# Kernel optimization log

Hardware: AMD Instinct MI355X
Metric: run time of the kernel (lower is better)

## Reference

```python
import jax, jax.numpy as jnp
import numpy as np

B, T, F, N = 262144, 3, 17, 8
EMBD = 32
DT = 0.2  # 25/5*0.04
EPS = 1e-8  # torch.cosine_similarity eps


def _mono(x, wi, bi, wo, bo):
    # monotonic_fun with increasing=False: relu(-Linear(x)) -> Linear
    h = jax.nn.relu(-(x @ wi.T + bi))  # (..., EMBD)
    return h @ wo.T + bo               # (..., 1)


def _cos(a, b):
    dot = jnp.sum(a * b, axis=-1)
    na = jnp.maximum(jnp.linalg.norm(a, axis=-1), EPS)
    nb = jnp.maximum(jnp.linalg.norm(b, axis=-1), EPS)
    return dot / (na * nb)


def _angle_clamp(vec, e, ang):
    # vec: (B,K,2), e: (B,2) -> keep forces within effective angle cone, sum over K
    keep = jnp.abs(_cos(e[:, None, :], vec)) > ang
    return jnp.sum(vec * keep[..., None], axis=1)


def setup_inputs() -> dict:
    key = jax.random.key(0)
    ks = jax.random.split(key, 8)
    ego = jax.random.normal(ks[0], (B, T, F), jnp.float32)
    ego = ego.at[:, :, 2:4].multiply(10.0)  # position scale
    nei = jax.random.normal(ks[1], (B, N, F), jnp.float32)
    nei = nei.at[:, :, 2:4].multiply(10.0).at[:, :, 4:6].multiply(0.1)
    border = jax.random.normal(ks[2], (4,), jnp.float32)
    attr_dest_para = jax.random.uniform(ks[3], (2,), jnp.float32) + 0.1  # relu(rand), keep away from 0 divisor
    eff_angle = jax.nn.sigmoid(jax.random.uniform(ks[4], (1,), jnp.float32))

    def mlp(k):
        k1, k2, k3, k4 = jax.random.split(k, 4)
        wi = jax.random.uniform(k1, (EMBD, 1), jnp.float32)      # clamped >= 0
        bi = jax.random.normal(k2, (EMBD,), jnp.float32) * 0.1
        wo = jax.random.uniform(k3, (1, EMBD), jnp.float32) * 0.1  # clamped >= 0
        bo = jax.random.normal(k4, (1,), jnp.float32) * 0.1
        return wi, bi, wo, bo

    an = mlp(ks[5])
    rn = mlp(ks[6])
    rb = mlp(ks[7])
    dl = mlp(jax.random.fold_in(key, 99))
    return dict(
        ego=ego, nei=nei, border=border,
        attr_dest_para=attr_dest_para, eff_angle=eff_angle,
        an_wi=an[0], an_bi=an[1], an_wo=an[2], an_bo=an[3],
        rn_wi=rn[0], rn_bi=rn[1], rn_wo=rn[2], rn_bo=rn[3],
        rb_wi=rb[0], rb_bi=rb[1], rb_wo=rb[2], rb_bo=rb[3],
        dl_wi=dl[0], dl_bi=dl[1], dl_wo=dl[2], dl_bo=dl[3],
    )


def reference(ego, nei, border, attr_dest_para, eff_angle,
              an_wi, an_bi, an_wo, an_bo,
              rn_wi, rn_bi, rn_wo, rn_bo,
              rb_wi, rb_bi, rb_wo, rb_bo,
              dl_wi, dl_bi, dl_wo, dl_bo):
    ego_last = ego[:, -1]  # (B,F)

    # --- attr_destination (desired_velocity=None branch) ---
    v34 = ego_last[:, 3:5]
    dv = jnp.stack([jnp.linalg.norm(v34, axis=-1),
                    jnp.zeros(ego.shape[0], ego.dtype)], axis=1)  # (B,2)
    f_dest = ((attr_dest_para[1] * dv - v34) / attr_dest_para[0])[:, None, :]  # (B,1,2)

    # --- attr_repu_neighbors ---
    r = nei[:, :, 2:4] - ego_last[:, None, 2:4]  # (B,N,2)
    mask = nei[:, :, 2:4] == 0                    # (B,N,2)
    r_norm = jnp.linalg.norm(r, axis=-1, keepdims=True)  # (B,N,1)

    # neighbor durality: quirky use of batch element 1, shared across batch
    ids_last = ego[1, -1, 8:-1]  # (8,) neighbor-id columns
    dur = jnp.zeros(N, ego.dtype)
    for t in range(ego.shape[1]):
        dur = dur + jnp.isin(ids_last, ego[1, t, 8:-1]).astype(ego.dtype)

    f_attr = _mono(r_norm, an_wi, an_bi, an_wo, an_bo) * r / r_norm \
             * _mono(dur[:, None], dl_wi, dl_bi, dl_wo, dl_bo)  # (B,N,2)*(N,1)
    f_attr = jnp.where(mask, 0.0, f_attr)

    v_nei = nei[:, :, 4:6]
    b = r_norm \
        + jnp.sum((r + v_nei * DT) ** 2, axis=-1, keepdims=True) \
        - jnp.sum((v_nei * DT) ** 2, axis=-1, keepdims=True)
    b = jnp.sqrt(b) / 2
    f_repu = _mono(b, rn_wi, rn_bi, rn_wo, rn_bo) * r / r_norm
    f_repu = jnp.where(mask, 0.0, f_repu)

    # --- repu_borders (select_lane = [0, -1]) ---
    rb_all = ego_last[:, 3, None] - border        # (B,4)
    rbv = jnp.stack([rb_all[:, 0], rb_all[:, -1]], axis=1)  # (B,2)
    rbn = jnp.abs(rbv)
    f_bor = _mono(rbn[..., None], rb_wi, rb_bi, rb_wo, rb_bo) * (rbv / rbn)[..., None]  # (B,2,1)
    f_bor = jnp.concatenate([jnp.zeros_like(f_bor), f_bor], axis=-1)  # (B,2,2): [0, fy]

    # --- angle clamp + integrate ---
    e = ego_last[:, 4:6]
    e = e / jnp.linalg.norm(e, axis=1, keepdims=True)
    a = (_angle_clamp(f_dest, e, eff_angle)
         + _angle_clamp(f_attr, e, eff_angle) + _angle_clamp(f_repu, e, eff_angle)
         + _angle_clamp(f_bor, e, eff_angle))
    v = ego_last[:, 2:4] + a * DT
    s = ego_last[:, :2] + v * DT
    return jnp.concatenate([s, v, a], axis=1)  # (B,6)
```

## Files before the change

### kernel.cpp

```cpp
#include <hip/hip_runtime.h>

#define DTC 0.2f
#define EPSC 1e-8f

__global__ void sfm_pre(const float* __restrict__ ego,
                        const float* __restrict__ dl_wi,
                        const float* __restrict__ dl_bi,
                        const float* __restrict__ dl_wo,
                        const float* __restrict__ dl_bo,
                        float* __restrict__ ws) {
    int t = threadIdx.x;
    int j = t >> 5, k = t & 31;
    const float* base = ego + 51;
    float idv = base[2 * 17 + 8 + j];
    float dur = 0.f;
    for (int tt = 0; tt < 3; ++tt) {
        bool f = false;
        for (int m = 0; m < 8; ++m) f = f || (idv == base[tt * 17 + 8 + m]);
        dur += f ? 1.f : 0.f;
    }
    float part = dl_wo[k] * fmaxf(0.f, -fmaf(dl_wi[k], dur, dl_bi[k]));
#pragma unroll
    for (int m = 1; m < 32; m <<= 1) part += __shfl_xor(part, m, 64);
    if (k == 0) ws[j] = part + dl_bo[0];
}

__global__ __launch_bounds__(256) void sfm_main(
    const float* __restrict__ ego, const float* __restrict__ nei,
    const float* __restrict__ border, const float* __restrict__ adp,
    const float* __restrict__ eang,
    const float* __restrict__ an_wi, const float* __restrict__ an_bi,
    const float* __restrict__ an_wo, const float* __restrict__ an_bo,
    const float* __restrict__ rn_wi, const float* __restrict__ rn_bi,
    const float* __restrict__ rn_wo, const float* __restrict__ rn_bo,
    const float* __restrict__ rb_wi, const float* __restrict__ rb_bi,
    const float* __restrict__ rb_wo, const float* __restrict__ rb_bo,
    const float* __restrict__ dlf,
    float* __restrict__ out, int Bn)
{
    __shared__ float sw[304];
    int t = threadIdx.x;
    if (t < 32) {
        sw[t]        = an_wi[t]; sw[32 + t]  = an_bi[t]; sw[64 + t]  = an_wo[t];
        sw[96 + t]   = rn_wi[t]; sw[128 + t] = rn_bi[t]; sw[160 + t] = rn_wo[t];
        sw[192 + t]  = rb_wi[t]; sw[224 + t] = rb_bi[t]; sw[256 + t] = rb_wo[t];
    }
    if (t >= 32 && t < 40) sw[288 + (t - 32)] = dlf[t - 32];
    if (t == 40) sw[296] = an_bo[0];
    if (t == 41) sw[297] = rn_bo[0];
    if (t == 42) sw[298] = rb_bo[0];
    if (t == 43) sw[299] = adp[0];
    if (t == 44) sw[300] = adp[1];
    if (t == 45) sw[301] = eang[0];
    if (t == 46) sw[302] = border[0];
    if (t == 47) sw[303] = border[3];
    __syncthreads();

    int l = t & 7;
    long long row = (long long)blockIdx.x * 32 + (t >> 3);
    if (row >= Bn) return;

    float egv = 0.f;
    if (l < 6) egv = ego[row * 51 + 34 + l];
    int lb = (t & 63) & ~7;
    float g0 = __shfl(egv, lb + 0, 64);
    float g1 = __shfl(egv, lb + 1, 64);
    float g2 = __shfl(egv, lb + 2, 64);
    float g3 = __shfl(egv, lb + 3, 64);
    float g4 = __shfl(egv, lb + 4, 64);
    float g5 = __shfl(egv, lb + 5, 64);

    const float* nr = nei + row * 136 + l * 17 + 2;
    float nx = nr[0], ny = nr[1], vx = nr[2], vy = nr[3];

    float Rx = nx - g2, Ry = ny - g3;
    float rr = sqrtf(Rx * Rx + Ry * Ry);
    float ax = fmaf(vx, DTC, Rx), ay = fmaf(vy, DTC, Ry);
    float wx = vx * DTC, wy = vy * DTC;
    float bb = sqrtf(rr + ax * ax + ay * ay - wx * wx - wy * wy) * 0.5f;

    float rb0 = g3 - sw[302], rb1 = g3 - sw[303];
    float rbn0 = fabsf(rb0), rbn1 = fabsf(rb1);

    float accA = 0.f, accR = 0.f;
#pragma unroll 8
    for (int k = 0; k < 32; ++k) {
        float h = fmaxf(0.f, -fmaf(sw[k], rr, sw[32 + k]));
        accA = fmaf(sw[64 + k], h, accA);
        float g = fmaxf(0.f, -fmaf(sw[96 + k], bb, sw[128 + k]));
        accR = fmaf(sw[160 + k], g, accR);
    }
    float pB0 = 0.f, pB1 = 0.f;
#pragma unroll
    for (int m = 0; m < 4; ++m) {
        int k = l + 8 * m;
        float bwi = sw[192 + k], bbi = sw[224 + k], bwo = sw[256 + k];
        pB0 = fmaf(bwo, fmaxf(0.f, -fmaf(bwi, rbn0, bbi)), pB0);
        pB1 = fmaf(bwo, fmaxf(0.f, -fmaf(bwi, rbn1, bbi)), pB1);
    }

    float an_bo_v = sw[296], rn_bo_v = sw[297], rb_bo_v = sw[298];
    float p0 = sw[299], p1 = sw[300], ang = sw[301];

    float elen = sqrtf(g4 * g4 + g5 * g5);
    float ex = g4 / elen, ey = g5 / elen;
    float na = fmaxf(sqrtf(ex * ex + ey * ey), EPSC);

    float axs = 0.f, ays = 0.f;
#define CLAMP_ADD(VX, VY)                                                   \
    {                                                                       \
        float _vx = (VX), _vy = (VY);                                       \
        float _nv = fmaxf(sqrtf(_vx * _vx + _vy * _vy), EPSC);              \
        float _c = (ex * _vx + ey * _vy) / (na * _nv);                      \
        if (fabsf(_c) > ang) { axs += _vx; ays += _vy; }                    \
    }

    float mfx = (nx == 0.f) ? 0.f : 1.f;
    float mfy = (ny == 0.f) ? 0.f : 1.f;

    {
        float coef = (accA + an_bo_v) / rr * sw[288 + l];
        CLAMP_ADD(coef * Rx * mfx, coef * Ry * mfy);
    }
    {
        float coef = (accR + rn_bo_v) / rr;
        CLAMP_ADD(coef * Rx * mfx, coef * Ry * mfy);
    }

#pragma unroll
    for (int m = 1; m < 8; m <<= 1) {
        axs += __shfl_xor(axs, m, 64);
        ays += __shfl_xor(ays, m, 64);
        pB0 += __shfl_xor(pB0, m, 64);
        pB1 += __shfl_xor(pB1, m, 64);
    }

    if (l == 0) {
        float dvn = sqrtf(g3 * g3 + g4 * g4);
        CLAMP_ADD((p1 * dvn - g3) / p0, -g4 / p0);
        float f0 = (pB0 + rb_bo_v) * (rb0 / rbn0);
        float f1 = (pB1 + rb_bo_v) * (rb1 / rbn1);
        CLAMP_ADD(0.f, f0);
        CLAMP_ADD(0.f, f1);

        float vxo = fmaf(axs, DTC, g2);
        float vyo = fmaf(ays, DTC, g3);
        float* op = out + row * 6;
        op[0] = fmaf(vxo, DTC, g0);
        op[1] = fmaf(vyo, DTC, g1);
        op[2] = vxo; op[3] = vyo;
        op[4] = axs; op[5] = ays;
    }
#undef CLAMP_ADD
}

extern "C" void kernel_launch(void* const* d_in, const int* in_sizes, int n_in,
                              void* d_out, int out_size, void* d_ws, size_t ws_size,
                              hipStream_t stream) {
    const float* ego    = (const float*)d_in[0];
    const float* nei    = (const float*)d_in[1];
    const float* border = (const float*)d_in[2];
    const float* adp    = (const float*)d_in[3];
    const float* eang   = (const float*)d_in[4];
    const float* an_wi  = (const float*)d_in[5];
    const float* an_bi  = (const float*)d_in[6];
    const float* an_wo  = (const float*)d_in[7];
    const float* an_bo  = (const float*)d_in[8];
    const float* rn_wi  = (const float*)d_in[9];
    const float* rn_bi  = (const float*)d_in[10];
    const float* rn_wo  = (const float*)d_in[11];
    const float* rn_bo  = (const float*)d_in[12];
    const float* rb_wi  = (const float*)d_in[13];
    const float* rb_bi  = (const float*)d_in[14];
    const float* rb_wo  = (const float*)d_in[15];
    const float* rb_bo  = (const float*)d_in[16];
    const float* dl_wi  = (const float*)d_in[17];
    const float* dl_bi  = (const float*)d_in[18];
    const float* dl_wo  = (const float*)d_in[19];
    const float* dl_bo  = (const float*)d_in[20];
    float* out = (float*)d_out;
    float* ws  = (float*)d_ws;

    int Bn = in_sizes[0] / (3 * 17);

    sfm_pre<<<1, 256, 0, stream>>>(ego, dl_wi, dl_bi, dl_wo, dl_bo, ws);

    int grid = (Bn + 31) / 32;
    sfm_main<<<grid, 256, 0, stream>>>(ego, nei, border, adp, eang,
                                       an_wi, an_bi, an_wo, an_bo,
                                       rn_wi, rn_bi, rn_wo, rn_bo,
                                       rb_wi, rb_bi, rb_wo, rb_bo,
                                       ws, out, Bn);
}
```

Before: 278.8 us.

## Replace 32-unit ReLU MLP loops with sorted-breakpoint piecewise-linear lookup

Each scalar-input monotone MLP is a piecewise-linear function of its input. A prologue kernel now computes the breakpoints -bi/wi, sorts them, and builds suffix sums of wi*wo and wo*bi into the workspace. The main kernel then evaluates each MLP with a 5-step binary search and one FMA instead of 32 ReLU-FMA iterations, and computes border forces on two lanes followed by a shuffle. This assumes wi > 0 so every unit is active for inputs below its breakpoint; a zero wi or a different sign would give wrong results. Results can also differ slightly from the reference because the sums are accumulated in a different order.

```diff
diff --git a/kernel.cpp b/kernel.cpp
--- a/kernel.cpp
+++ b/kernel.cpp
@@ -3,57 +3,98 @@
 #define DTC 0.2f
 #define EPSC 1e-8f
 
-__global__ void sfm_pre(const float* __restrict__ ego,
-                        const float* __restrict__ dl_wi,
-                        const float* __restrict__ dl_bi,
-                        const float* __restrict__ dl_wo,
-                        const float* __restrict__ dl_bo,
-                        float* __restrict__ ws) {
+
+__global__ __launch_bounds__(128) void sfm_pre(
+    const float* __restrict__ ego,
+    const float* __restrict__ an_wi, const float* __restrict__ an_bi, const float* __restrict__ an_wo,
+    const float* __restrict__ rn_wi, const float* __restrict__ rn_bi, const float* __restrict__ rn_wo,
+    const float* __restrict__ rb_wi, const float* __restrict__ rb_bi, const float* __restrict__ rb_wo,
+    const float* __restrict__ dl_wi, const float* __restrict__ dl_bi,
+    const float* __restrict__ dl_wo, const float* __restrict__ dl_bo,
+    float* __restrict__ ws)
+{
+    __shared__ float tk[96], wiwo[96], wobi[96], skn[96], ssw[96], ssb[96];
     int t = threadIdx.x;
-    int j = t >> 5, k = t & 31;
-    const float* base = ego + 51;
-    float idv = base[2 * 17 + 8 + j];
-    float dur = 0.f;
-    for (int tt = 0; tt < 3; ++tt) {
-        bool f = false;
-        for (int m = 0; m < 8; ++m) f = f || (idv == base[tt * 17 + 8 + m]);
-        dur += f ? 1.f : 0.f;
-    }
-    float part = dl_wo[k] * fmaxf(0.f, -fmaf(dl_wi[k], dur, dl_bi[k]));
-#pragma unroll
-    for (int m = 1; m < 32; m <<= 1) part += __shfl_xor(part, m, 64);
-    if (k == 0) ws[j] = part + dl_bo[0];
+    if (t < 96) {
+        int f = t >> 5, k = t & 31;
+        const float* wip = (f == 0) ? an_wi : ((f == 1) ? rn_wi : rb_wi);
+        const float* bip = (f == 0) ? an_bi : ((f == 1) ? rn_bi : rb_bi);
+        const float* wop = (f == 0) ? an_wo : ((f == 1) ? rn_wo : rb_wo);
+        float wi = wip[k], bi = bip[k], wo = wop[k];
+        tk[t]   = -bi / wi;
+        wiwo[t] = wi * wo;
+        wobi[t] = wo * bi;
+    }
+    __syncthreads();
+    if (t < 96) {
+        int f = t >> 5, k = t & 31;
+        float my = tk[t];
+        int rank = 0;
+        for (int m = 0; m < 32; ++m) {
+            float o = tk[f * 32 + m];
+            rank += (o < my || (o == my && m < k)) ? 1 : 0;
+        }
+        skn[f * 32 + rank] = my;
+        ssw[f * 32 + rank] = wiwo[t];
+        ssb[f * 32 + rank] = wobi[t];
+    }
+    __syncthreads();
+    if (t < 96) {
+        int f = t >> 5, p = t & 31;
+        float sw_ = 0.f, sb_ = 0.f;
+        for (int m = p; m < 32; ++m) { sw_ += ssw[f * 32 + m]; sb_ += ssb[f * 32 + m]; }
+        int base = 16 + f * 112;
+        ws[base + p]      = skn[f * 32 + p];
+        ws[base + 32 + p] = sw_;
+        ws[base + 65 + p] = sb_;
+        if (p == 0) { ws[base + 64] = 0.f; ws[base + 97] = 0.f; }
+    }
+    if (t >= 96 && t < 104) {
+        int j = t - 96;
+        const float* base = ego + 51;
+        float idv = base[2 * 17 + 8 + j];
+        float dur = 0.f;
+        for (int tt = 0; tt < 3; ++tt) {
+            bool fo = false;
+            for (int m = 0; m < 8; ++m) fo = fo || (idv == base[tt * 17 + 8 + m]);
+            dur += fo ? 1.f : 0.f;
+        }
+        float acc = 0.f;
+        for (int k = 0; k < 32; ++k)
+            acc = fmaf(dl_wo[k], fmaxf(0.f, -fmaf(dl_wi[k], dur, dl_bi[k])), acc);
+        ws[j] = acc + dl_bo[0];
+    }
+}
+
+__device__ __forceinline__ float mono_eval(const float* __restrict__ kn, float x) {
+    int i = (kn[15] <= x) ? 16 : 0;
+    i += (kn[i + 7] <= x) ? 8 : 0;
+    i += (kn[i + 3] <= x) ? 4 : 0;
+    i += (kn[i + 1] <= x) ? 2 : 0;
+    i += (kn[i] <= x) ? 1 : 0;
+    return -fmaf(kn[32 + i], x, kn[65 + i]);
 }
 
 __global__ __launch_bounds__(256) void sfm_main(
     const float* __restrict__ ego, const float* __restrict__ nei,
     const float* __restrict__ border, const float* __restrict__ adp,
     const float* __restrict__ eang,
-    const float* __restrict__ an_wi, const float* __restrict__ an_bi,
-    const float* __restrict__ an_wo, const float* __restrict__ an_bo,
-    const float* __restrict__ rn_wi, const float* __restrict__ rn_bi,
-    const float* __restrict__ rn_wo, const float* __restrict__ rn_bo,
-    const float* __restrict__ rb_wi, const float* __restrict__ rb_bi,
-    const float* __restrict__ rb_wo, const float* __restrict__ rb_bo,
-    const float* __restrict__ dlf,
+    const float* __restrict__ an_bo, const float* __restrict__ rn_bo,
+    const float* __restrict__ rb_bo,
+    const float* __restrict__ wsrc,
     float* __restrict__ out, int Bn)
 {
-    __shared__ float sw[304];
+    __shared__ float sw[360];
     int t = threadIdx.x;
-    if (t < 32) {
-        sw[t]        = an_wi[t]; sw[32 + t]  = an_bi[t]; sw[64 + t]  = an_wo[t];
-        sw[96 + t]   = rn_wi[t]; sw[128 + t] = rn_bi[t]; sw[160 + t] = rn_wo[t];
-        sw[192 + t]  = rb_wi[t]; sw[224 + t] = rb_bi[t]; sw[256 + t] = rb_wo[t];
-    }
-    if (t >= 32 && t < 40) sw[288 + (t - 32)] = dlf[t - 32];
-    if (t == 40) sw[296] = an_bo[0];
-    if (t == 41) sw[297] = rn_bo[0];
-    if (t == 42) sw[298] = rb_bo[0];
-    if (t == 43) sw[299] = adp[0];
-    if (t == 44) sw[300] = adp[1];
-    if (t == 45) sw[301] = eang[0];
-    if (t == 46) sw[302] = border[0];
-    if (t == 47) sw[303] = border[3];
+    for (int i = t; i < 352; i += 256) sw[i] = wsrc[i];
+    if (t == 0) sw[352] = an_bo[0];
+    if (t == 1) sw[353] = rn_bo[0];
+    if (t == 2) sw[354] = rb_bo[0];
+    if (t == 3) sw[355] = adp[0];
+    if (t == 4) sw[356] = adp[1];
+    if (t == 5) sw[357] = eang[0];
+    if (t == 6) sw[358] = border[0];
+    if (t == 7) sw[359] = border[3];
     __syncthreads();
 
     int l = t & 7;
@@ -79,28 +120,18 @@
     float wx = vx * DTC, wy = vy * DTC;
     float bb = sqrtf(rr + ax * ax + ay * ay - wx * wx - wy * wy) * 0.5f;
 
-    float rb0 = g3 - sw[302], rb1 = g3 - sw[303];
+    float an_bo_v = sw[352], rn_bo_v = sw[353], rb_bo_v = sw[354];
+    float p0 = sw[355], p1 = sw[356], ang = sw[357];
+    float rb0 = g3 - sw[358], rb1 = g3 - sw[359];
     float rbn0 = fabsf(rb0), rbn1 = fabsf(rb1);
 
-    float accA = 0.f, accR = 0.f;
-#pragma unroll 8
-    for (int k = 0; k < 32; ++k) {
-        float h = fmaxf(0.f, -fmaf(sw[k], rr, sw[32 + k]));
-        accA = fmaf(sw[64 + k], h, accA);
-        float g = fmaxf(0.f, -fmaf(sw[96 + k], bb, sw[128 + k]));
-        accR = fmaf(sw[160 + k], g, accR);
-    }
-    float pB0 = 0.f, pB1 = 0.f;
-#pragma unroll
-    for (int m = 0; m < 4; ++m) {
-        int k = l + 8 * m;
-        float bwi = sw[192 + k], bbi = sw[224 + k], bwo = sw[256 + k];
-        pB0 = fmaf(bwo, fmaxf(0.f, -fmaf(bwi, rbn0, bbi)), pB0);
-        pB1 = fmaf(bwo, fmaxf(0.f, -fmaf(bwi, rbn1, bbi)), pB1);
-    }
-
-    float an_bo_v = sw[296], rn_bo_v = sw[297], rb_bo_v = sw[298];
-    float p0 = sw[299], p1 = sw[300], ang = sw[301];
+    float fA = mono_eval(sw + 16, rr) + an_bo_v;
+    float fR = mono_eval(sw + 128, bb) + rn_bo_v;
+    float xb = (l == 1) ? rbn1 : rbn0;
+    float vB = 0.f;
+    if (l < 2) vB = mono_eval(sw + 240, xb) + rb_bo_v;
+    float vB0 = __shfl(vB, lb + 0, 64);
+    float vB1 = __shfl(vB, lb + 1, 64);
 
     float elen = sqrtf(g4 * g4 + g5 * g5);
     float ex = g4 / elen, ey = g5 / elen;
@@ -119,11 +150,11 @@
     float mfy = (ny == 0.f) ? 0.f : 1.f;
 
     {
-        float coef = (accA + an_bo_v) / rr * sw[288 + l];
+        float coef = fA / rr * sw[l];
         CLAMP_ADD(coef * Rx * mfx, coef * Ry * mfy);
     }
     {
-        float coef = (accR + rn_bo_v) / rr;
+        float coef = fR / rr;
         CLAMP_ADD(coef * Rx * mfx, coef * Ry * mfy);
     }
 
@@ -131,17 +162,13 @@
     for (int m = 1; m < 8; m <<= 1) {
         axs += __shfl_xor(axs, m, 64);
         ays += __shfl_xor(ays, m, 64);
-        pB0 += __shfl_xor(pB0, m, 64);
-        pB1 += __shfl_xor(pB1, m, 64);
     }
 
     if (l == 0) {
         float dvn = sqrtf(g3 * g3 + g4 * g4);
         CLAMP_ADD((p1 * dvn - g3) / p0, -g4 / p0);
-        float f0 = (pB0 + rb_bo_v) * (rb0 / rbn0);
-        float f1 = (pB1 + rb_bo_v) * (rb1 / rbn1);
-        CLAMP_ADD(0.f, f0);
-        CLAMP_ADD(0.f, f1);
+        CLAMP_ADD(0.f, vB0 * (rb0 / rbn0));
+        CLAMP_ADD(0.f, vB1 * (rb1 / rbn1));
 
         float vxo = fmaf(axs, DTC, g2);
         float vyo = fmaf(ays, DTC, g3);
@@ -183,12 +210,14 @@
 
     int Bn = in_sizes[0] / (3 * 17);
 
-    sfm_pre<<<1, 256, 0, stream>>>(ego, dl_wi, dl_bi, dl_wo, dl_bo, ws);
+    sfm_pre<<<1, 128, 0, stream>>>(ego,
+                                   an_wi, an_bi, an_wo,
+                                   rn_wi, rn_bi, rn_wo,
+                                   rb_wi, rb_bi, rb_wo,
+                                   dl_wi, dl_bi, dl_wo, dl_bo, ws);
 
     int grid = (Bn + 31) / 32;
     sfm_main<<<grid, 256, 0, stream>>>(ego, nei, border, adp, eang,
-                                       an_wi, an_bi, an_wo, an_bo,
-                                       rn_wi, rn_bi, rn_wo, rn_bo,
-                                       rb_wi, rb_bi, rb_wo, rb_bo,
+                                       an_bo, rn_bo, rb_bo,
                                        ws, out, Bn);
 }
```

After: 278.8 us (median of 2 runs). No clear change (-0.0%).
